# Optimization experiments

Measured on AMD Instinct MI355X. Metric: run time of the kernel, lower is better.

The kernel has to match this reference:

```python
import jax, jax.numpy as jnp
import numpy as np

# Model dims (Mamba2-2.7B-like)
B_SZ = 1; SEQ = 2048; HID = 2048
INTER = 4096; N_STATE = 128; N_GROUPS = 1; NH = 64; HD = 64
K_CONV = 4; CHUNK = 256
GN = N_GROUPS * N_STATE            # 128
CONV_DIM = INTER + 2 * GN          # 4352
D_IN = 2 * INTER + 2 * GN + NH     # 8512
EPS = 1e-5


def setup_inputs() -> dict:
    key = jax.random.key(0)
    ks = jax.random.split(key, 8)
    return {
        "hidden_states": jax.random.normal(ks[0], (B_SZ, SEQ, HID), jnp.float32),
        "W_in": jax.random.normal(ks[1], (HID, D_IN), jnp.float32) * 0.02,
        "conv_w": jax.random.normal(ks[2], (CONV_DIM, K_CONV), jnp.float32) * 0.2,
        "conv_b": jax.random.normal(ks[3], (CONV_DIM,), jnp.float32) * 0.1,
        "dt_bias": jax.random.uniform(ks[4], (NH,), jnp.float32, -4.0, 0.0),
        "A": -jnp.exp(jax.random.uniform(ks[5], (NH,), jnp.float32, -1.0, 1.0)),
        "D": jnp.ones((NH,), jnp.float32),
        "norm_weight": jnp.ones((INTER,), jnp.float32),
        "W_out": jax.random.normal(ks[6], (INTER, HID), jnp.float32) * 0.02,
    }


def reference(hidden_states, W_in, conv_w, conv_b, dt_bias, A, D, norm_weight, W_out):
    b, S, _ = hidden_states.shape
    # in_proj and split: gate [inter], x/B/C [conv_dim], dt [num_heads]
    proj = hidden_states @ W_in
    gate, xBC, dt = jnp.split(proj, [INTER, INTER + CONV_DIM], axis=-1)
    dt = jax.nn.softplus(dt + dt_bias)  # [b,S,NH]

    # causal depthwise conv1d + SiLU (kernel K, left-padded)
    xp = jnp.pad(xBC, ((0, 0), (K_CONV - 1, 0), (0, 0)))
    conv = conv_b
    for k in range(K_CONV):  # tiny fixed loop over kernel taps
        conv = conv + conv_w[:, k] * xp[:, k:k + S, :]
    xBC = jax.nn.silu(conv)

    x, Bm, Cm = jnp.split(xBC, [INTER, INTER + GN], axis=-1)
    L = CHUNK; nc = S // L
    x_c = x.reshape(b, nc, L, NH, HD)
    rep = NH // N_GROUPS
    B_c = jnp.repeat(Bm.reshape(b, nc, L, N_GROUPS, N_STATE), rep, axis=3)  # bclhn
    C_c = jnp.repeat(Cm.reshape(b, nc, L, N_GROUPS, N_STATE), rep, axis=3)
    dt_c = dt.reshape(b, nc, L, NH)

    dA = dt_c * A                      # [b,c,l,h]  (A < 0)
    cA = jnp.cumsum(dA, axis=2)        # within-chunk cumulative log-decay
    cAt = jnp.transpose(cA, (0, 1, 3, 2))  # [b,c,h,l]

    # intra-chunk: causal decay matrix, (C B^T) masked, weighted by dt
    diff = cAt[..., :, None] - cAt[..., None, :]          # [b,c,h,l,s]
    tril = jnp.tril(jnp.ones((L, L), bool))
    Lmat = jnp.exp(jnp.where(tril, diff, -jnp.inf))
    CB = jnp.einsum('bclhn,bcshn->bchls', C_c, B_c)
    M = CB * Lmat * jnp.transpose(dt_c, (0, 1, 3, 2))[:, :, :, None, :]
    Y_intra = jnp.einsum('bchls,bcshp->bclhp', M, x_c)

    # per-chunk end state contributions
    decay_states = jnp.exp(cA[:, :, -1:, :] - cA)          # [b,c,l,h]
    states = jnp.einsum('bclh,bclhn,bclhp->bchpn', decay_states * dt_c, B_c, x_c)
    chunk_decay = jnp.exp(cA[:, :, -1, :])                 # [b,c,h]

    def step(carry, inp):
        d, st = inp
        new = carry * d[..., None, None] + st
        return new, carry  # emit state entering the chunk

    _, prev = jax.lax.scan(step, jnp.zeros((b, NH, HD, N_STATE), states.dtype),
                           (jnp.moveaxis(chunk_decay, 1, 0), jnp.moveaxis(states, 1, 0)))
    prev = jnp.moveaxis(prev, 0, 1)                        # [b,c,h,p,n]

    Y_inter = jnp.einsum('bclhn,bclh,bchpn->bclhp', C_c, jnp.exp(cA), prev)
    Y = Y_intra + Y_inter + x_c * D[:, None]               # skip D*x per head

    y = Y.reshape(b, S, INTER)
    # gated RMSNorm in fp32
    z = y.astype(jnp.float32) * jax.nn.silu(gate.astype(jnp.float32))
    var = jnp.mean(z * z, axis=-1, keepdims=True)
    z = z * jax.lax.rsqrt(var + EPS) * norm_weight
    return z @ W_out
```

## Files before the change

### kernel.cpp

```cpp
#include <hip/hip_runtime.h>

typedef __bf16 bf16_t;
typedef bf16_t bf16x8 __attribute__((ext_vector_type(8)));
typedef float f32x4 __attribute__((ext_vector_type(4)));
typedef unsigned short u16;
typedef u16 u16x8 __attribute__((ext_vector_type(8)));
typedef u16 u16x4 __attribute__((ext_vector_type(4)));

#define SEQ   2048
#define HID   2048
#define INTER 4096
#define NH    64
#define HD    64
#define CONVD 4352
#define DIN   8512
#define LDP   8576L
#define CHNK  256
#define NC    8

__device__ __forceinline__ u16 f2bf(float f) {
  union { float f; unsigned u; } a; a.f = f;
  return (u16)((a.u + 0x7fffu + ((a.u >> 16) & 1u)) >> 16);
}
__device__ __forceinline__ float bf2f(u16 u) {
  union { unsigned u; float f; } a; a.u = ((unsigned)u) << 16;
  return a.f;
}

__device__ __forceinline__ void gl2lds16(const void* g, void* l) {
  auto gp = reinterpret_cast<__attribute__((address_space(1))) void*>(
      (unsigned long long)g);
  auto lp = reinterpret_cast<__attribute__((address_space(3))) void*>(
      (unsigned)(unsigned long long)l);
  __builtin_amdgcn_global_load_lds(gp, lp, 16, 0, 0);
}

__device__ __forceinline__ bf16x8 ds128(unsigned addr) {
  bf16x8 r;
  asm volatile("ds_read_b128 %0, %1" : "=v"(r) : "v"(addr));
  return r;
}

__global__ __launch_bounds__(256) void cvt_bf16(const float* __restrict__ s,
                                                u16* __restrict__ d, int n4) {
  int i = blockIdx.x * 256 + threadIdx.x;
  if (i < n4) {
    f32x4 v = ((const f32x4*)s)[i];
    u16x4 r;
#pragma unroll
    for (int k = 0; k < 4; ++k) r[k] = f2bf(v[k]);
    ((u16x4*)d)[i] = r;
  }
}

__global__ void transpose_bf16(const float* __restrict__ src, u16* __restrict__ dst,
                               int R, int Cc) {
  __shared__ float t[32][33];
  int n0 = blockIdx.x * 32, k0 = blockIdx.y * 32;
  int tx = threadIdx.x, ty = threadIdx.y;
  for (int i = ty; i < 32; i += 8) {
    int n = n0 + tx;
    t[i][tx] = (n < Cc) ? src[(long)(k0 + i) * Cc + n] : 0.f;
  }
  __syncthreads();
  for (int i = ty; i < 32; i += 8)
    dst[(long)(n0 + i) * R + k0 + tx] = f2bf(t[tx][i]);
}

__global__ __launch_bounds__(256, 2) void gemm_bt(const u16* __restrict__ A,
                                                  const u16* __restrict__ Bt,
                                                  float* __restrict__ C,
                                                  int N, int lda, int Klen,
                                                  long zstride) {
  __shared__ __align__(16) u16 As[128 * 64];
  __shared__ __align__(16) u16 Bs[128 * 64];
  const int kz = blockIdx.z;
  A  += (long)kz * Klen;
  Bt += (long)kz * Klen;
  C  += (long)kz * zstride;
  const int nb = gridDim.x * gridDim.y;
  const int id = blockIdx.x + gridDim.x * blockIdx.y;
  const int s = (id & 7) * (nb >> 3) + (id >> 3);
  const long bm = s & 15;
  const long bn = s >> 4;

  const int tid = threadIdx.x;
  const int lane = tid & 63;
  const int w = tid >> 6;
  const int wm = w >> 1, wn = w & 1;

  f32x4 acc[4][4];
#pragma unroll
  for (int i = 0; i < 4; ++i)
#pragma unroll
    for (int j = 0; j < 4; ++j) acc[i][j] = (f32x4){0.f, 0.f, 0.f, 0.f};

  const int srr = lane >> 3;
  const int sc8 = ((lane & 7) ^ srr) * 8;
  const u16* Agw = A + (bm * 128 + w * 8 + srr) * (long)lda + sc8;
  const u16* Bgw = Bt + (bn * 128 + w * 8 + srr) * (long)lda + sc8;
  u16* ldA = As + w * 512 + lane * 8;
  u16* ldB = Bs + w * 512 + lane * 8;
  const int fr = lane & 15, q = lane >> 4;
  const int fx = (fr & 7) << 3;

  for (int k0 = 0; k0 < Klen; k0 += 64) {
    __syncthreads();
#pragma unroll
    for (int t = 0; t < 4; ++t) {
      gl2lds16(Agw + k0 + (long)t * 32 * lda, ldA + t * 2048);
      gl2lds16(Bgw + k0 + (long)t * 32 * lda, ldB + t * 2048);
    }
    __builtin_amdgcn_s_waitcnt(0);
    __syncthreads();
#pragma unroll
    for (int ks = 0; ks < 2; ++ks) {
      bf16x8 af[4], bfv[4];
#pragma unroll
      for (int i = 0; i < 4; ++i)
        af[i] = *(const bf16x8*)(As + ((wm * 64 + i * 16 + fr) << 6) +
                                 ((((ks << 2) + q) << 3) ^ fx));
#pragma unroll
      for (int j = 0; j < 4; ++j)
        bfv[j] = *(const bf16x8*)(Bs + ((wn * 64 + j * 16 + fr) << 6) +
                                  ((((ks << 2) + q) << 3) ^ fx));
#pragma unroll
      for (int i = 0; i < 4; ++i)
#pragma unroll
        for (int j = 0; j < 4; ++j)
          acc[i][j] = __builtin_amdgcn_mfma_f32_16x16x32_bf16(af[i], bfv[j], acc[i][j], 0, 0, 0);
    }
  }
  const int cr = (lane >> 4) * 4;
  const int cc = lane & 15;
#pragma unroll
  for (int i = 0; i < 4; ++i)
#pragma unroll
    for (int j = 0; j < 4; ++j) {
      long r = bm * 128 + wm * 64 + i * 16 + cr;
      long cidx = bn * 128 + wn * 64 + j * 16 + cc;
      float* cp = C + r * (long)N + cidx;
#pragma unroll
      for (int t = 0; t < 4; ++t) cp[(long)t * N] = acc[i][j][t];
    }
}

#define MFMA16(ACC, AF, BF)                                                    \
  _Pragma("unroll") for (int i_ = 0; i_ < 4; ++i_)                             \
  _Pragma("unroll") for (int j_ = 0; j_ < 2; ++j_) {                           \
    ACC[i_][j_] = __builtin_amdgcn_mfma_f32_16x16x32_bf16(                     \
        AF[i_][0], BF[j_][0], ACC[i_][j_], 0, 0, 0);                           \
    ACC[i_][j_] = __builtin_amdgcn_mfma_f32_16x16x32_bf16(                     \
        AF[i_][1], BF[j_][1], ACC[i_][j_], 0, 0, 0);                           \
  }

#define LDAF(DST, SLOT)                                                        \
  {                                                                            \
    unsigned ab_ = (unsigned)(unsigned long long)(&Abuf[SLOT][0]);             \
    _Pragma("unroll") for (int i_ = 0; i_ < 4; ++i_) {                         \
      unsigned ro_ = ab_ + (((wm * 64 + i_ * 16 + fr) << 6) << 1);             \
      DST[i_][0] = ds128(ro_ + (ke0 << 1));                                    \
      DST[i_][1] = ds128(ro_ + (ke1 << 1));                                    \
    }                                                                          \
  }

#define LDBF(DST, SLOT)                                                        \
  {                                                                            \
    unsigned bb_ = (unsigned)(unsigned long long)(&Bbuf[SLOT][0]);             \
    _Pragma("unroll") for (int j_ = 0; j_ < 2; ++j_) {                         \
      unsigned ro_ = bb_ + (((wn * 32 + j_ * 16 + fr) << 6) << 1);             \
      DST[j_][0] = ds128(ro_ + (ke0 << 1));                                    \
      DST[j_][1] = ds128(ro_ + (ke1 << 1));                                    \
    }                                                                          \
  }

#define STAGE(G, HO, KO, SLOT, BUF)                                            \
  {                                                                            \
    const u16* g_ = (G) + (HO) + (KO);                                         \
    gl2lds16(g_ + off1, BUF[SLOT] + lo1);                                      \
    gl2lds16(g_ + off2, BUF[SLOT] + lo2);                                      \
  }

#define PH_FENCE()                                                             \
  asm volatile("s_waitcnt lgkmcnt(0)" ::: "memory");                           \
  __builtin_amdgcn_sched_barrier(0);

__global__ __launch_bounds__(512, 2) void gemm256(const u16* __restrict__ A,
                                                  const u16* __restrict__ Bt,
                                                  float* __restrict__ C,
                                                  int N, int lda, int Klen,
                                                  long zstride) {
  __shared__ __align__(16) u16 Abuf[4][128 * 64];
  __shared__ __align__(16) u16 Bbuf[4][128 * 64];

  const int kz = blockIdx.z;
  A  += (long)kz * Klen;
  Bt += (long)kz * Klen;
  C  += (long)kz * zstride;

  const int nb = gridDim.x * gridDim.y;
  const int id = blockIdx.x + gridDim.x * blockIdx.y;
  const int s = (id & 7) * (nb >> 3) + (id >> 3);
  const long bm = s & 7;
  const long bn = s >> 3;

  const int tid = threadIdx.x;
  const int lane = tid & 63;
  const int w = tid >> 6;
  const int wm = w >> 2;
  const int wn = w & 3;
  const int fr = lane & 15, q = lane >> 4;
  const int ke0 = (q ^ (fr & 7)) << 3;
  const int ke1 = ((4 + q) ^ (fr & 7)) << 3;

  const int sr1 = (w << 4) + (lane >> 3);
  const int sr2 = sr1 + 8;
  const int kcp = lane & 7;
  const long off1 = (long)sr1 * lda + ((kcp ^ (sr1 & 7)) << 3);
  const long off2 = (long)sr2 * lda + ((kcp ^ (sr2 & 7)) << 3);
  const int lo1 = (w << 10) + (lane << 3);
  const int lo2 = lo1 + 512;
  const long h128 = 128L * lda;

  const u16* gA = A + bm * 256 * lda;
  const u16* gB = Bt + bn * 256 * lda;

  f32x4 acc00[4][2], acc01[4][2], acc10[4][2], acc11[4][2];
#pragma unroll
  for (int i = 0; i < 4; ++i)
#pragma unroll
    for (int j = 0; j < 2; ++j) {
      acc00[i][j] = (f32x4){0.f, 0.f, 0.f, 0.f};
      acc01[i][j] = (f32x4){0.f, 0.f, 0.f, 0.f};
      acc10[i][j] = (f32x4){0.f, 0.f, 0.f, 0.f};
      acc11[i][j] = (f32x4){0.f, 0.f, 0.f, 0.f};
    }

  const int NT = Klen >> 6;

  STAGE(gA, 0L, 0L, 0, Abuf);
  STAGE(gB, 0L, 0L, 0, Bbuf);
  STAGE(gB, h128, 0L, 1, Bbuf);
  STAGE(gA, h128, 0L, 1, Abuf);
  STAGE(gA, 0L, 64L, 2, Abuf);
  STAGE(gB, 0L, 64L, 2, Bbuf);
  STAGE(gB, h128, 64L, 3, Bbuf);
  STAGE(gA, h128, 64L, 3, Abuf);
  asm volatile("s_waitcnt vmcnt(8)" ::: "memory");
  __builtin_amdgcn_s_barrier();

  for (int T = 0; T < NT; ++T) {
    const int t2 = (T << 1) & 3;
    const int t2p1 = (t2 + 1) & 3;
    const long kT2 = (long)(T + 2) << 6;
    const bool g2 = (T + 2 < NT);
    bf16x8 a0[4][2], a1[4][2], b0[2][2], b1[2][2];

    LDAF(a0, t2);
    LDBF(b0, t2);
    asm volatile("s_waitcnt lgkmcnt(8)" ::: "memory");
    __builtin_amdgcn_s_barrier();
    PH_FENCE();
    __builtin_amdgcn_s_setprio(1);
    MFMA16(acc00, a0, b0);
    __builtin_amdgcn_s_setprio(0);
    __builtin_amdgcn_s_barrier();

    LDBF(b1, t2p1);
    if (g2) STAGE(gA, 0L, kT2, t2, Abuf);
    __builtin_amdgcn_s_barrier();
    PH_FENCE();
    __builtin_amdgcn_s_setprio(1);
    MFMA16(acc01, a0, b1);
    __builtin_amdgcn_s_setprio(0);
    __builtin_amdgcn_s_barrier();

    LDAF(a1, t2p1);
    if (g2) STAGE(gB, 0L, kT2, t2, Bbuf);
    __builtin_amdgcn_s_barrier();
    PH_FENCE();
    __builtin_amdgcn_s_setprio(1);
    MFMA16(acc10, a1, b0);
    __builtin_amdgcn_s_setprio(0);
    __builtin_amdgcn_s_barrier();

    if (g2) {
      STAGE(gB, h128, kT2, t2p1, Bbuf);
      STAGE(gA, h128, kT2, t2p1, Abuf);
    }
    __builtin_amdgcn_s_barrier();
    PH_FENCE();
    __builtin_amdgcn_s_setprio(1);
    MFMA16(acc11, a1, b1);
    __builtin_amdgcn_s_setprio(0);
    if (g2)
      asm volatile("s_waitcnt vmcnt(8)" ::: "memory");
    else
      asm volatile("s_waitcnt vmcnt(0)" ::: "memory");
    __builtin_amdgcn_s_barrier();
  }

  const int cr = (lane >> 4) << 2;
  const int cc = lane & 15;
  const long r0 = bm * 256 + wm * 64 + cr;
  const long c0 = bn * 256 + wn * 32 + cc;
#define CWRITE(ACC, QA, QB)                                                    \
  _Pragma("unroll") for (int i_ = 0; i_ < 4; ++i_)                             \
  _Pragma("unroll") for (int j_ = 0; j_ < 2; ++j_) {                           \
    long r_ = r0 + (QA)*128 + i_ * 16;                                         \
    long c_ = c0 + (QB)*128 + j_ * 16;                                         \
    if (c_ < N) {                                                              \
      float* cp_ = C + r_ * (long)N + c_;                                      \
      _Pragma("unroll") for (int t_ = 0; t_ < 4; ++t_)                         \
          cp_[(long)t_ * N] = ACC[i_][j_][t_];                                 \
    }                                                                          \
  }
  CWRITE(acc00, 0, 0)
  CWRITE(acc01, 0, 1)
  CWRITE(acc10, 1, 0)
  CWRITE(acc11, 1, 1)
#undef CWRITE
}

__global__ __launch_bounds__(256) void add4_kernel(const float* __restrict__ a,
                                                   float* __restrict__ o) {
  int i = blockIdx.x * 256 + threadIdx.x;
  f32x4 r = ((const f32x4*)a)[i];
  r += ((const f32x4*)(a + 4194304L))[i];
  r += ((const f32x4*)(a + 8388608L))[i];
  r += ((const f32x4*)(a + 12582912L))[i];
  ((f32x4*)o)[i] = r;
}

__global__ __launch_bounds__(256) void strip_add(const float* __restrict__ a,
                                                 float* __restrict__ proj) {
  int g = blockIdx.x * 256 + threadIdx.x;
  int r = g / 96, c4 = g - r * 96;
  f32x4 v = ((const f32x4*)a)[g];
  v += ((const f32x4*)(a + 786432L))[g];
  v += ((const f32x4*)(a + 1572864L))[g];
  v += ((const f32x4*)(a + 2359296L))[g];
  ((f32x4*)(proj + (long)r * LDP + 8192))[c4] = v;
}

__global__ __launch_bounds__(256) void conv_silu_t(const float* __restrict__ proj,
                                                   const float* __restrict__ cw,
                                                   const float* __restrict__ cb,
                                                   u16* __restrict__ xbf,
                                                   u16* __restrict__ xT) {
  __shared__ float ld[35][33];
  __shared__ u16 tt[32][34];
  const int c0 = blockIdx.x * 32, t0 = blockIdx.y * 32;
  const int tx = threadIdx.x & 31, ty = threadIdx.x >> 5;
  for (int i = ty; i < 35; i += 8) {
    int t = t0 - 3 + i;
    ld[i][tx] = (t >= 0) ? proj[(long)t * LDP + INTER + c0 + tx] : 0.f;
  }
  const int c = c0 + tx;
  const float w0 = cw[c * 4 + 0], w1 = cw[c * 4 + 1], w2 = cw[c * 4 + 2],
              w3 = cw[c * 4 + 3], bias = cb[c];
  __syncthreads();
  for (int i = ty; i < 32; i += 8) {
    float a = bias + w0 * ld[i][tx] + w1 * ld[i + 1][tx] + w2 * ld[i + 2][tx] +
              w3 * ld[i + 3][tx];
    u16 v = f2bf(a / (1.f + __expf(-a)));
    xbf[(long)(t0 + i) * CONVD + c] = v;
    tt[i][tx] = v;
  }
  __syncthreads();
  if (c0 < 4224) {
    for (int i = ty; i < 32; i += 8)
      xT[(long)(c0 + i) * 2048 + t0 + tx] = tt[tx][i];
  }
}

__global__ __launch_bounds__(256) void dt_cumsum(const float* __restrict__ proj,
                                                 const float* __restrict__ dtb,
                                                 const float* __restrict__ A,
                                                 float* __restrict__ dt2,
                                                 float* __restrict__ cA2) {
  __shared__ float sc[256];
  int c = blockIdx.x, h = blockIdx.y, l = threadIdx.x;
  float v = proj[(long)(c * 256 + l) * LDP + 8448 + h] + dtb[h];
  float sp = (v > 20.f) ? v : log1pf(__expf(v));
  dt2[h * 2048 + c * 256 + l] = sp;
  sc[l] = sp * A[h];
  __syncthreads();
  for (int off = 1; off < 256; off <<= 1) {
    float t = (l >= off) ? sc[l - off] : 0.f;
    __syncthreads();
    sc[l] += t;
    __syncthreads();
  }
  cA2[h * 2048 + c * 256 + l] = sc[l];
}

__global__ __launch_bounds__(256, 2) void cb_gemm(const u16* __restrict__ xbf,
                                                  float* __restrict__ CB) {
  __shared__ __align__(16) u16 As[128 * 32];
  __shared__ __align__(16) u16 Bs[128 * 32];
  const int tid = threadIdx.x;
  const int lane = tid & 63;
  const int w = tid >> 6;
  const int wm = w >> 1, wn = w & 1;
  const int bm = blockIdx.y, bn = blockIdx.x, c = blockIdx.z;

  f32x4 acc[4][4];
#pragma unroll
  for (int i = 0; i < 4; ++i)
#pragma unroll
    for (int j = 0; j < 4; ++j) acc[i][j] = (f32x4){0.f, 0.f, 0.f, 0.f};

  const int sr = w * 32 + (lane >> 2);
  const int sc = ((lane & 3) ^ ((lane >> 2) & 3)) * 8;
  const u16* Ag = xbf + (long)(c * 256 + bm * 128) * CONVD + 4224;
  const u16* Bg = xbf + (long)(c * 256 + bn * 128) * CONVD + 4096;
  u16* lA0 = As + w * 1024 + lane * 8;
  u16* lA1 = As + w * 1024 + 512 + lane * 8;
  u16* lB0 = Bs + w * 1024 + lane * 8;
  u16* lB1 = Bs + w * 1024 + 512 + lane * 8;
  const int fr = lane & 15, q = lane >> 4;
  const int pc = ((q ^ (fr & 3)) << 3);

  for (int k0 = 0; k0 < 128; k0 += 32) {
    __syncthreads();
    const u16* a0 = Ag + (long)sr * CONVD + k0 + sc;
    const u16* b0 = Bg + (long)sr * CONVD + k0 + sc;
    gl2lds16(a0, lA0);
    gl2lds16(a0 + 16L * CONVD, lA1);
    gl2lds16(b0, lB0);
    gl2lds16(b0 + 16L * CONVD, lB1);
    __builtin_amdgcn_s_waitcnt(0);
    __syncthreads();
    bf16x8 af[4], bfv[4];
#pragma unroll
    for (int i = 0; i < 4; ++i)
      af[i] = *(const bf16x8*)(As + ((wm * 64 + i * 16 + fr) << 5) + pc);
#pragma unroll
    for (int j = 0; j < 4; ++j)
      bfv[j] = *(const bf16x8*)(Bs + ((wn * 64 + j * 16 + fr) << 5) + pc);
#pragma unroll
    for (int i = 0; i < 4; ++i)
#pragma unroll
      for (int j = 0; j < 4; ++j)
        acc[i][j] = __builtin_amdgcn_mfma_f32_16x16x32_bf16(af[i], bfv[j], acc[i][j], 0, 0, 0);
  }
  const int cr = (lane >> 4) * 4;
  const int cc = lane & 15;
  float* Cc = CB + (long)c * 65536;
#pragma unroll
  for (int i = 0; i < 4; ++i)
#pragma unroll
    for (int j = 0; j < 4; ++j) {
      int r = bm * 128 + wm * 64 + i * 16 + cr;
      int cidx = bn * 128 + wn * 64 + j * 16 + cc;
      float* cp = Cc + (long)r * 256 + cidx;
#pragma unroll
      for (int t = 0; t < 4; ++t) cp[t * 256] = acc[i][j][t];
    }
}

#define LDM 72
__global__ __launch_bounds__(256) void states_kernel(const u16* __restrict__ xT,
                                                     const float* __restrict__ dt2,
                                                     const float* __restrict__ cA2,
                                                     float* __restrict__ stT) {
  __shared__ __align__(16) u16 Ms[128 * LDM];
  __shared__ __align__(16) u16 Xs[64 * LDM];
  __shared__ float wl[256];
  const int c = blockIdx.x, h = blockIdx.y;
  const int tid = threadIdx.x;
  const int lane = tid & 63, w = tid >> 6;
  const int fr = lane & 15, q = lane >> 4;
  {
    float calast = cA2[h * 2048 + c * 256 + 255];
    float ca = cA2[h * 2048 + c * 256 + tid];
    wl[tid] = __expf(calast - ca) * dt2[h * 2048 + c * 256 + tid];
  }
  f32x4 acc[2][4];
#pragma unroll
  for (int i = 0; i < 2; ++i)
#pragma unroll
    for (int j = 0; j < 4; ++j) acc[i][j] = (f32x4){0.f, 0.f, 0.f, 0.f};

  const int lc8 = (tid & 7) * 8;
  const int rn = tid >> 3;
  __syncthreads();

  for (int kt = 0; kt < 4; ++kt) {
    __syncthreads();
#pragma unroll
    for (int r = 0; r < 4; ++r) {
      int n = rn + 32 * r;
      u16x8 raw = *(const u16x8*)(xT + (long)(4096 + n) * 2048 + c * 256 + kt * 64 + lc8);
      union { u16 u[8]; bf16x8 v; } pk;
#pragma unroll
      for (int u = 0; u < 8; ++u)
        pk.u[u] = f2bf(bf2f(raw[u]) * wl[kt * 64 + lc8 + u]);
      *(bf16x8*)(Ms + n * LDM + lc8) = pk.v;
    }
#pragma unroll
    for (int r = 0; r < 2; ++r) {
      int p = rn + 32 * r;
      *(bf16x8*)(Xs + p * LDM + lc8) =
          *(const bf16x8*)(xT + (long)(h * 64 + p) * 2048 + c * 256 + kt * 64 + lc8);
    }
    __syncthreads();
#pragma unroll
    for (int ks = 0; ks < 64; ks += 32) {
      bf16x8 af[2], xf[4];
#pragma unroll
      for (int i = 0; i < 2; ++i)
        af[i] = *(const bf16x8*)(Ms + (w * 32 + i * 16 + fr) * LDM + ks + q * 8);
#pragma unroll
      for (int j = 0; j < 4; ++j)
        xf[j] = *(const bf16x8*)(Xs + (j * 16 + fr) * LDM + ks + q * 8);
#pragma unroll
      for (int i = 0; i < 2; ++i)
#pragma unroll
        for (int j = 0; j < 4; ++j)
          acc[i][j] = __builtin_amdgcn_mfma_f32_16x16x32_bf16(af[i], xf[j], acc[i][j], 0, 0, 0);
    }
  }
  const int cr = (lane >> 4) * 4;
  const int cc = lane & 15;
  float* outp = stT + (long)(c * 64 + h) * 8192;
#pragma unroll
  for (int i = 0; i < 2; ++i)
#pragma unroll
    for (int j = 0; j < 4; ++j) {
      int n = w * 32 + i * 16 + cr;
      int p = j * 16 + cc;
#pragma unroll
      for (int t = 0; t < 4; ++t) outp[(n + t) * 64 + p] = acc[i][j][t];
    }
}

__global__ __launch_bounds__(256) void scan_kernel(const float* __restrict__ stT,
                                                   const float* __restrict__ cA2,
                                                   float* __restrict__ prevT) {
  int id = blockIdx.x * 256 + threadIdx.x;
  int h = id >> 13;
  float acc = 0.f;
#pragma unroll
  for (int c = 0; c < NC; ++c) {
    prevT[(long)c * 524288 + id] = acc;
    float cd = __expf(cA2[h * 2048 + c * 256 + 255]);
    acc = acc * cd + stT[(long)c * 524288 + id];
  }
}

__global__ __launch_bounds__(256) void ssm_y_kernel(const u16* __restrict__ xbf,
                                                    const u16* __restrict__ xT,
                                                    const float* __restrict__ dt2,
                                                    const float* __restrict__ cA2,
                                                    const float* __restrict__ CB,
                                                    const float* __restrict__ prevT,
                                                    const float* __restrict__ Dp,
                                                    u16* __restrict__ Y) {
  __shared__ __align__(16) u16 Ms[256 * LDM];
  __shared__ __align__(16) u16 Xt[64 * LDM];
  __shared__ float cas[256];
  __shared__ float dts[256];
  const int c = blockIdx.x, h = blockIdx.y;
  const int tid = threadIdx.x;
  const int lane = tid & 63;
  const int w = tid >> 6;
  const int fr = lane & 15, q = lane >> 4;

  cas[tid] = cA2[h * 2048 + c * 256 + tid];
  dts[tid] = dt2[h * 2048 + c * 256 + tid];

  f32x4 acc[4][4];
#pragma unroll
  for (int i = 0; i < 4; ++i)
#pragma unroll
    for (int j = 0; j < 4; ++j) acc[i][j] = (f32x4){0.f, 0.f, 0.f, 0.f};

  const int sg = (tid & 7) * 8;
  const int lb = tid >> 3;
  const int xp = tid & 63;
  const int xq = tid >> 6;

  __syncthreads();

  for (int kt = 0; kt < 6; ++kt) {
    __syncthreads();
    if (kt < 4) {
      const int s0 = kt * 64;
      f32x4 e0 = *(const f32x4*)&cas[s0 + sg];
      f32x4 e1 = *(const f32x4*)&cas[s0 + sg + 4];
      f32x4 d0 = *(const f32x4*)&dts[s0 + sg];
      f32x4 d1 = *(const f32x4*)&dts[s0 + sg + 4];
#pragma unroll
      for (int k = 0; k < 8; ++k) {
        const int l = lb + 32 * k;
        const float cal = cas[l];
        const float* cb = CB + (long)c * 65536 + (long)l * 256 + s0 + sg;
        f32x4 c0 = *(const f32x4*)cb;
        f32x4 c1 = *(const f32x4*)(cb + 4);
        union { u16 u[8]; bf16x8 v; } pk;
#pragma unroll
        for (int u = 0; u < 8; ++u) {
          int s = s0 + sg + u;
          float cv = (u < 4) ? c0[u] : c1[u - 4];
          float cs = (u < 4) ? e0[u] : e1[u - 4];
          float dv = (u < 4) ? d0[u] : d1[u - 4];
          float m = (s <= l) ? cv * __expf(cal - cs) * dv : 0.f;
          pk.u[u] = f2bf(m);
        }
        *(bf16x8*)(Ms + l * LDM + sg) = pk.v;
      }
#pragma unroll
      for (int r = 0; r < 2; ++r) {
        int p = (tid >> 3) + 32 * r;
        *(bf16x8*)(Xt + p * LDM + sg) =
            *(const bf16x8*)(xT + (long)(h * 64 + p) * 2048 + c * 256 + s0 + sg);
      }
    } else {
      const int n0 = (kt - 4) * 64;
#pragma unroll
      for (int k = 0; k < 8; ++k) {
        const int l = lb + 32 * k;
        const float ea = __expf(cas[l]);
        u16x8 raw = *(const u16x8*)(xbf + (long)(c * 256 + l) * CONVD + 4224 + n0 + sg);
        union { u16 u[8]; bf16x8 v; } pk;
#pragma unroll
        for (int u = 0; u < 8; ++u) pk.u[u] = f2bf(ea * bf2f(raw[u]));
        *(bf16x8*)(Ms + l * LDM + sg) = pk.v;
      }
      const float* pT = prevT + (long)(c * 64 + h) * 8192;
#pragma unroll
      for (int half = 0; half < 2; ++half) {
        const int nb2 = xq * 16 + half * 8;
        union { u16 u[8]; bf16x8 v; } pk;
#pragma unroll
        for (int u = 0; u < 8; ++u) pk.u[u] = f2bf(pT[(n0 + nb2 + u) * 64 + xp]);
        *(bf16x8*)(Xt + xp * LDM + nb2) = pk.v;
      }
    }
    __syncthreads();
#pragma unroll
    for (int ks = 0; ks < 64; ks += 32) {
      bf16x8 af[4], bfv[4];
#pragma unroll
      for (int i = 0; i < 4; ++i)
        af[i] = *(const bf16x8*)(Ms + (w * 64 + i * 16 + fr) * LDM + ks + q * 8);
#pragma unroll
      for (int j = 0; j < 4; ++j)
        bfv[j] = *(const bf16x8*)(Xt + (j * 16 + fr) * LDM + ks + q * 8);
#pragma unroll
      for (int i = 0; i < 4; ++i)
#pragma unroll
        for (int j = 0; j < 4; ++j)
          acc[i][j] = __builtin_amdgcn_mfma_f32_16x16x32_bf16(af[i], bfv[j], acc[i][j], 0, 0, 0);
    }
  }

  const int cr = (lane >> 4) * 4;
  const int cc = lane & 15;
  const float dh = Dp[h];
#pragma unroll
  for (int i = 0; i < 4; ++i)
#pragma unroll
    for (int j = 0; j < 4; ++j) {
      const int p = j * 16 + cc;
#pragma unroll
      for (int t = 0; t < 4; ++t) {
        const int row = w * 64 + i * 16 + cr + t;
        const float xv = bf2f(xbf[(long)(c * 256 + row) * CONVD + h * 64 + p]);
        Y[(long)(c * 256 + row) * 4096 + h * 64 + p] = f2bf(acc[i][j][t] + dh * xv);
      }
    }
}

__global__ __launch_bounds__(256) void rmsnorm_kernel(const u16* __restrict__ Y,
                                                      const float* __restrict__ proj,
                                                      const float* __restrict__ nw,
                                                      u16* __restrict__ zbf) {
  __shared__ float red[256];
  int t = blockIdx.x, tid = threadIdx.x;
  const u16* y = Y + (long)t * 4096;
  const float* g = proj + (long)t * LDP;
  float zv[16];
  float s = 0.f;
#pragma unroll
  for (int k = 0; k < 16; ++k) {
    int i = tid + k * 256;
    float gv = g[i];
    float z = bf2f(y[i]) * (gv / (1.f + __expf(-gv)));
    zv[k] = z;
    s += z * z;
  }
  red[tid] = s;
  __syncthreads();
  if (tid < 128) red[tid] += red[tid + 128];
  __syncthreads();
  if (tid < 64) {
    float v = red[tid] + red[tid + 64];
    v += __shfl_down(v, 32);
    v += __shfl_down(v, 16);
    v += __shfl_down(v, 8);
    v += __shfl_down(v, 4);
    v += __shfl_down(v, 2);
    v += __shfl_down(v, 1);
    if (tid == 0) red[0] = v;
  }
  __syncthreads();
  float scale = rsqrtf(red[0] * (1.f / 4096.f) + 1e-5f);
#pragma unroll
  for (int k = 0; k < 16; ++k) {
    int i = tid + k * 256;
    zbf[(long)t * 4096 + i] = f2bf(zv[k] * scale * nw[i]);
  }
}

extern "C" void kernel_launch(void* const* d_in, const int* in_sizes, int n_in,
                              void* d_out, int out_size, void* d_ws, size_t ws_size,
                              hipStream_t stream) {
  const float* hidden = (const float*)d_in[0];
  const float* Win    = (const float*)d_in[1];
  const float* convw  = (const float*)d_in[2];
  const float* convb  = (const float*)d_in[3];
  const float* dtb    = (const float*)d_in[4];
  const float* Ap     = (const float*)d_in[5];
  const float* Dp     = (const float*)d_in[6];
  const float* nw     = (const float*)d_in[7];
  const float* Wout   = (const float*)d_in[8];
  float* out = (float*)d_out;
  char* ws = (char*)d_ws;

  u16*   hb    = (u16*)(ws + 0);
  u16*   WinT  = (u16*)(ws + 8388608L);
  float* proj  = (float*)(ws + 43515904L);
  u16*   WoutT = (u16*)(ws + 113770496L);
  u16*   xbf   = (u16*)(ws + 130547712L);
  u16*   xT    = (u16*)(ws + 148373504L);
  float* dt2   = (float*)(ws + 165675008L);
  float* cA2   = (float*)(ws + 166199296L);
  float* CBv   = (float*)(ws + 166723584L);
  float* stT   = (float*)(ws + 168820736L);
  float* prevT = (float*)(ws + 185597952L);
  u16*   zbf   = (u16*)(ws + 202375168L);
  u16*   Y     = (u16*)(ws + 0);
  float* Cp    = (float*)(ws + 43515904L);
  float* Cs    = (float*)(ws + 168820736L);

  cvt_bf16<<<4096, 256, 0, stream>>>(hidden, hb, 1048576);
  transpose_bf16<<<dim3(268, 64), dim3(32, 8), 0, stream>>>(Win, WinT, 2048, 8512);
  transpose_bf16<<<dim3(64, 128), dim3(32, 8), 0, stream>>>(Wout, WoutT, 4096, 2048);
  gemm256<<<dim3(32, 8, 1), 512, 0, stream>>>(hb, WinT, proj, 8576, 2048, 2048, 0L);
  gemm_bt<<<dim3(3, 16, 4), 256, 0, stream>>>(hb, WinT + 8192L * 2048, Cs,
                                              384, 2048, 512, 786432L);
  strip_add<<<768, 256, 0, stream>>>(Cs, proj);
  conv_silu_t<<<dim3(136, 64), 256, 0, stream>>>(proj, convw, convb, xbf, xT);
  dt_cumsum<<<dim3(8, 64), 256, 0, stream>>>(proj, dtb, Ap, dt2, cA2);
  cb_gemm<<<dim3(2, 2, 8), 256, 0, stream>>>(xbf, CBv);
  states_kernel<<<dim3(8, 64), 256, 0, stream>>>(xT, dt2, cA2, stT);
  scan_kernel<<<2048, 256, 0, stream>>>(stT, cA2, prevT);
  ssm_y_kernel<<<dim3(8, 64), 256, 0, stream>>>(xbf, xT, dt2, cA2, CBv, prevT, Dp, Y);
  rmsnorm_kernel<<<2048, 256, 0, stream>>>(Y, proj, nw, zbf);
  gemm256<<<dim3(8, 8, 4), 512, 0, stream>>>(zbf, WoutT, Cp, 2048, 4096, 1024, 4194304L);
  add4_kernel<<<4096, 256, 0, stream>>>(Cp, out);
}
```

Before: 407.7 us.

## Store in_proj gate/x in bf16 and vectorize weight transpose

The main in_proj GEMM now writes its gate and xBC columns as bf16 into a compact 8192-wide buffer, while the B/C/dt strip stays fp32 in a separate buffer. The conv, dt and rmsnorm consumers read from these two buffers. This roughly halves the bytes written and re-read for the large projection output, at the cost of rounding the gate and x activations to bf16. The weight transpose kernel is also rewritten with 64x64 tiles, vector float4 loads and 16-byte bf16 stores to cut memory transactions.

New measurement: 389.2 us. 1.05x faster.

```diff
diff --git a/kernel.cpp b/kernel.cpp
--- a/kernel.cpp
+++ b/kernel.cpp
@@ -14,7 +14,6 @@
 #define HD    64
 #define CONVD 4352
 #define DIN   8512
-#define LDP   8576L
 #define CHNK  256
 #define NC    8
 
@@ -53,18 +52,43 @@
   }
 }
 
-__global__ void transpose_bf16(const float* __restrict__ src, u16* __restrict__ dst,
-                               int R, int Cc) {
-  __shared__ float t[32][33];
-  int n0 = blockIdx.x * 32, k0 = blockIdx.y * 32;
-  int tx = threadIdx.x, ty = threadIdx.y;
-  for (int i = ty; i < 32; i += 8) {
-    int n = n0 + tx;
-    t[i][tx] = (n < Cc) ? src[(long)(k0 + i) * Cc + n] : 0.f;
+__global__ __launch_bounds__(256) void transpose_bf16(const float* __restrict__ src,
+                                                      u16* __restrict__ dst,
+                                                      int R, int Cc) {
+  __shared__ u16 t[64][72];
+  const int n0 = blockIdx.x * 64, k0 = blockIdx.y * 64;
+  const int tx = threadIdx.x & 15;
+  const int ty = threadIdx.x >> 4;
+  if (n0 + 63 < Cc) {
+#pragma unroll
+    for (int j = 0; j < 4; ++j) {
+      int k = ty + j * 16;
+      f32x4 v = *(const f32x4*)(src + (long)(k0 + k) * Cc + n0 + tx * 4);
+#pragma unroll
+      for (int e = 0; e < 4; ++e) t[tx * 4 + e][k] = f2bf(v[e]);
+    }
+  } else {
+#pragma unroll
+    for (int j = 0; j < 4; ++j) {
+      int k = ty + j * 16;
+#pragma unroll
+      for (int e = 0; e < 4; ++e) {
+        int n = n0 + tx * 4 + e;
+        t[tx * 4 + e][k] = (n < Cc) ? f2bf(src[(long)(k0 + k) * Cc + n]) : (u16)0;
+      }
+    }
   }
   __syncthreads();
-  for (int i = ty; i < 32; i += 8)
-    dst[(long)(n0 + i) * R + k0 + tx] = f2bf(t[tx][i]);
+  const int cg = threadIdx.x & 7;
+  const int r0 = threadIdx.x >> 3;
+#pragma unroll
+  for (int j = 0; j < 2; ++j) {
+    int row = r0 + j * 32;
+    u16x8 o;
+#pragma unroll
+    for (int e = 0; e < 8; ++e) o[e] = t[row][cg * 8 + e];
+    *(u16x8*)(dst + (long)(n0 + row) * R + k0 + cg * 8) = o;
+  }
 }
 
 __global__ __launch_bounds__(256, 2) void gemm_bt(const u16* __restrict__ A,
@@ -185,9 +209,10 @@
   asm volatile("s_waitcnt lgkmcnt(0)" ::: "memory");                           \
   __builtin_amdgcn_sched_barrier(0);
 
+template <int BFOUT>
 __global__ __launch_bounds__(512, 2) void gemm256(const u16* __restrict__ A,
                                                   const u16* __restrict__ Bt,
-                                                  float* __restrict__ C,
+                                                  void* __restrict__ Cv,
                                                   int N, int lda, int Klen,
                                                   long zstride) {
   __shared__ __align__(16) u16 Abuf[4][128 * 64];
@@ -196,7 +221,7 @@
   const int kz = blockIdx.z;
   A  += (long)kz * Klen;
   Bt += (long)kz * Klen;
-  C  += (long)kz * zstride;
+  const long czoff = (long)kz * zstride;
 
   const int nb = gridDim.x * gridDim.y;
   const int id = blockIdx.x + gridDim.x * blockIdx.y;
@@ -310,9 +335,13 @@
     long r_ = r0 + (QA)*128 + i_ * 16;                                         \
     long c_ = c0 + (QB)*128 + j_ * 16;                                         \
     if (c_ < N) {                                                              \
-      float* cp_ = C + r_ * (long)N + c_;                                      \
-      _Pragma("unroll") for (int t_ = 0; t_ < 4; ++t_)                         \
-          cp_[(long)t_ * N] = ACC[i_][j_][t_];                                 \
+      long base_ = czoff + r_ * (long)N + c_;                                  \
+      _Pragma("unroll") for (int t_ = 0; t_ < 4; ++t_) {                       \
+        if (BFOUT)                                                             \
+          ((u16*)Cv)[base_ + (long)t_ * N] = f2bf(ACC[i_][j_][t_]);            \
+        else                                                                   \
+          ((float*)Cv)[base_ + (long)t_ * N] = ACC[i_][j_][t_];                \
+      }                                                                        \
     }                                                                          \
   }
   CWRITE(acc00, 0, 0)
@@ -333,17 +362,17 @@
 }
 
 __global__ __launch_bounds__(256) void strip_add(const float* __restrict__ a,
-                                                 float* __restrict__ proj) {
+                                                 float* __restrict__ ps) {
   int g = blockIdx.x * 256 + threadIdx.x;
-  int r = g / 96, c4 = g - r * 96;
   f32x4 v = ((const f32x4*)a)[g];
   v += ((const f32x4*)(a + 786432L))[g];
   v += ((const f32x4*)(a + 1572864L))[g];
   v += ((const f32x4*)(a + 2359296L))[g];
-  ((f32x4*)(proj + (long)r * LDP + 8192))[c4] = v;
-}
-
-__global__ __launch_bounds__(256) void conv_silu_t(const float* __restrict__ proj,
+  ((f32x4*)ps)[g] = v;
+}
+
+__global__ __launch_bounds__(256) void conv_silu_t(const u16* __restrict__ pb,
+                                                   const float* __restrict__ ps,
                                                    const float* __restrict__ cw,
                                                    const float* __restrict__ cb,
                                                    u16* __restrict__ xbf,
@@ -352,9 +381,15 @@
   __shared__ u16 tt[32][34];
   const int c0 = blockIdx.x * 32, t0 = blockIdx.y * 32;
   const int tx = threadIdx.x & 31, ty = threadIdx.x >> 5;
+  const bool mainreg = (c0 < 4096);
   for (int i = ty; i < 35; i += 8) {
     int t = t0 - 3 + i;
-    ld[i][tx] = (t >= 0) ? proj[(long)t * LDP + INTER + c0 + tx] : 0.f;
+    float v = 0.f;
+    if (t >= 0) {
+      if (mainreg) v = bf2f(pb[(long)t * 8192 + 4096 + c0 + tx]);
+      else         v = ps[(long)t * 384 + (c0 - 4096) + tx];
+    }
+    ld[i][tx] = v;
   }
   const int c = c0 + tx;
   const float w0 = cw[c * 4 + 0], w1 = cw[c * 4 + 1], w2 = cw[c * 4 + 2],
@@ -374,14 +409,14 @@
   }
 }
 
-__global__ __launch_bounds__(256) void dt_cumsum(const float* __restrict__ proj,
+__global__ __launch_bounds__(256) void dt_cumsum(const float* __restrict__ ps,
                                                  const float* __restrict__ dtb,
                                                  const float* __restrict__ A,
                                                  float* __restrict__ dt2,
                                                  float* __restrict__ cA2) {
   __shared__ float sc[256];
   int c = blockIdx.x, h = blockIdx.y, l = threadIdx.x;
-  float v = proj[(long)(c * 256 + l) * LDP + 8448 + h] + dtb[h];
+  float v = ps[(long)(c * 256 + l) * 384 + 256 + h] + dtb[h];
   float sp = (v > 20.f) ? v : log1pf(__expf(v));
   dt2[h * 2048 + c * 256 + l] = sp;
   sc[l] = sp * A[h];
@@ -675,19 +710,19 @@
 }
 
 __global__ __launch_bounds__(256) void rmsnorm_kernel(const u16* __restrict__ Y,
-                                                      const float* __restrict__ proj,
+                                                      const u16* __restrict__ pb,
                                                       const float* __restrict__ nw,
                                                       u16* __restrict__ zbf) {
   __shared__ float red[256];
   int t = blockIdx.x, tid = threadIdx.x;
   const u16* y = Y + (long)t * 4096;
-  const float* g = proj + (long)t * LDP;
+  const u16* g = pb + (long)t * 8192;
   float zv[16];
   float s = 0.f;
 #pragma unroll
   for (int k = 0; k < 16; ++k) {
     int i = tid + k * 256;
-    float gv = g[i];
+    float gv = bf2f(g[i]);
     float z = bf2f(y[i]) * (gv / (1.f + __expf(-gv)));
     zv[k] = z;
     s += z * z;
@@ -732,7 +767,8 @@
 
   u16*   hb    = (u16*)(ws + 0);
   u16*   WinT  = (u16*)(ws + 8388608L);
-  float* proj  = (float*)(ws + 43515904L);
+  u16*   pb    = (u16*)(ws + 43515904L);
+  float* ps    = (float*)(ws + 77070336L);
   u16*   WoutT = (u16*)(ws + 113770496L);
   u16*   xbf   = (u16*)(ws + 130547712L);
   u16*   xT    = (u16*)(ws + 148373504L);
@@ -747,19 +783,19 @@
   float* Cs    = (float*)(ws + 168820736L);
 
   cvt_bf16<<<4096, 256, 0, stream>>>(hidden, hb, 1048576);
-  transpose_bf16<<<dim3(268, 64), dim3(32, 8), 0, stream>>>(Win, WinT, 2048, 8512);
-  transpose_bf16<<<dim3(64, 128), dim3(32, 8), 0, stream>>>(Wout, WoutT, 4096, 2048);
-  gemm256<<<dim3(32, 8, 1), 512, 0, stream>>>(hb, WinT, proj, 8576, 2048, 2048, 0L);
+  transpose_bf16<<<dim3(134, 32), 256, 0, stream>>>(Win, WinT, 2048, 8512);
+  transpose_bf16<<<dim3(32, 64), 256, 0, stream>>>(Wout, WoutT, 4096, 2048);
+  gemm256<1><<<dim3(32, 8, 1), 512, 0, stream>>>(hb, WinT, pb, 8192, 2048, 2048, 0L);
   gemm_bt<<<dim3(3, 16, 4), 256, 0, stream>>>(hb, WinT + 8192L * 2048, Cs,
                                               384, 2048, 512, 786432L);
-  strip_add<<<768, 256, 0, stream>>>(Cs, proj);
-  conv_silu_t<<<dim3(136, 64), 256, 0, stream>>>(proj, convw, convb, xbf, xT);
-  dt_cumsum<<<dim3(8, 64), 256, 0, stream>>>(proj, dtb, Ap, dt2, cA2);
+  strip_add<<<768, 256, 0, stream>>>(Cs, ps);
+  conv_silu_t<<<dim3(136, 64), 256, 0, stream>>>(pb, ps, convw, convb, xbf, xT);
+  dt_cumsum<<<dim3(8, 64), 256, 0, stream>>>(ps, dtb, Ap, dt2, cA2);
   cb_gemm<<<dim3(2, 2, 8), 256, 0, stream>>>(xbf, CBv);
   states_kernel<<<dim3(8, 64), 256, 0, stream>>>(xT, dt2, cA2, stT);
   scan_kernel<<<2048, 256, 0, stream>>>(stT, cA2, prevT);
   ssm_y_kernel<<<dim3(8, 64), 256, 0, stream>>>(xbf, xT, dt2, cA2, CBv, prevT, Dp, Y);
-  rmsnorm_kernel<<<2048, 256, 0, stream>>>(Y, proj, nw, zbf);
-  gemm256<<<dim3(8, 8, 4), 512, 0, stream>>>(zbf, WoutT, Cp, 2048, 4096, 1024, 4194304L);
+  rmsnorm_kernel<<<2048, 256, 0, stream>>>(Y, pb, nw, zbf);
+  gemm256<0><<<dim3(8, 8, 4), 512, 0, stream>>>(zbf, WoutT, Cp, 2048, 4096, 1024, 4194304L);
   add4_kernel<<<4096, 256, 0, stream>>>(Cp, out);
 }
```
